# Optimization experiments

Hardware: AMD Instinct MI355X
Metric: run time of the kernel (lower is better)

The kernel has to match this reference:

```python
import jax, jax.numpy as jnp
import numpy as np

B, T, D = 16, 2048, 1024
TT = T - 2            # tokens after stripping BOS/EOS
WORD_EVERY = 3        # a word starts every 3 BPE tokens
MAX_WORDS = TT // WORD_EVERY  # 682
NUM_MUTEX, NUM_BIN = 64, 32


def setup_inputs() -> dict:
    key = jax.random.key(0)
    ks = jax.random.split(key, 7)
    features = jax.random.normal(ks[0], (B, T, D), dtype=jnp.float32)
    word_starts = jnp.zeros((B, TT), dtype=jnp.int32).at[:, ::WORD_EVERY].set(1)
    s = 1.0 / np.sqrt(D)
    dense_w = jax.random.normal(ks[1], (D, D), dtype=jnp.float32) * s
    dense_b = jax.random.normal(ks[2], (D,), dtype=jnp.float32) * 0.01
    out_w = jax.random.normal(ks[3], (NUM_MUTEX, D), dtype=jnp.float32) * s
    out_b = jax.random.normal(ks[4], (NUM_MUTEX,), dtype=jnp.float32) * 0.01
    bin_w = jax.random.normal(ks[5], (NUM_BIN, D + NUM_MUTEX), dtype=jnp.float32) * s
    bin_b = jax.random.normal(ks[6], (NUM_BIN,), dtype=jnp.float32) * 0.01
    return {"features": features, "word_starts": word_starts,
            "dense_w": dense_w, "dense_b": dense_b,
            "out_w": out_w, "out_b": out_b,
            "bin_w": bin_w, "bin_b": bin_b,
            "max_words": MAX_WORDS}


def _word_features(features, word_starts, max_words):
    # strip BOS/EOS
    x = features[:, 1:-1]                                  # [B, TT, D]
    b, tt, d = x.shape
    seg = jnp.cumsum(word_starts, axis=1) - 1              # word id per token; -1 before first start
    valid = seg >= 0
    flat_seg = seg + jnp.arange(b, dtype=seg.dtype)[:, None] * max_words
    overflow = b * max_words                               # dump invalid tokens into extra bucket
    flat_seg = jnp.where(valid, flat_seg, overflow).reshape(-1)
    sums = jax.ops.segment_sum(x.reshape(-1, d), flat_seg,
                               num_segments=b * max_words + 1)[:-1]
    counts = jax.ops.segment_sum(jnp.ones((b * tt,), dtype=x.dtype), flat_seg,
                                 num_segments=b * max_words + 1)[:-1]
    sums = sums.reshape(b, max_words, d)
    counts = counts.reshape(b, max_words, 1)
    # torch code initializes word_features to ONES; empty slots stay 1.0
    return jnp.where(counts > 0, sums, jnp.ones((), dtype=x.dtype))


def reference(features, word_starts, dense_w, dense_b, out_w, out_b, bin_w, bin_b, max_words):
    wf = _word_features(features, word_starts, max_words)   # [B, MW, D]
    # dropout p=0 (eval) -> identity
    h = jnp.tanh(jnp.einsum('bwd,ed->bwe', wf, dense_w) + dense_b)
    word_class_logits = jnp.einsum('bwd,cd->bwc', h, out_w) + out_b
    cat = jnp.concatenate((word_class_logits, h), axis=-1)  # [B, MW, Cm+D]
    binary_logits = jnp.einsum('bwd,cd->bwc', cat, bin_w) + bin_b
    return (word_class_logits, binary_logits)
```

## Files before the change

### kernel.cpp

```cpp
#include <hip/hip_runtime.h>
#include <stdint.h>

#define B_   16
#define T_   2048
#define D_   1024
#define TT_  2046
#define W_   682
#define BW_  (B_ * W_)
#define NMUT 64
#define NBIN 32

typedef __attribute__((ext_vector_type(8))) short s8b;
typedef __attribute__((ext_vector_type(4))) float f32x4;

__device__ inline short f2bf(float f) {
    uint32_t u = __builtin_bit_cast(uint32_t, f);
    u += 0x7FFFu + ((u >> 16) & 1u);
    return (short)(u >> 16);
}

__device__ inline void gload_lds16(const void* g, void* l) {
    __builtin_amdgcn_global_load_lds(
        (const __attribute__((address_space(1))) uint32_t*)g,
        (__attribute__((address_space(3))) uint32_t*)l, 16, 0, 0);
}

__global__ __launch_bounds__(256) void k_bounds(const int* __restrict__ ws,
                                                int* __restrict__ starts,
                                                int* __restrict__ nwords) {
    int b   = blockIdx.x;
    int tid = threadIdx.x;
    const int* row = ws + (size_t)b * TT_;

    int vals[8], incl[8];
    int p = 0;
    int t0 = tid * 8;
#pragma unroll
    for (int i = 0; i < 8; ++i) {
        int t = t0 + i;
        int v = (t < TT_) ? row[t] : 0;
        vals[i] = v;
        p += v;
        incl[i] = p;
    }
    int tot = p;

    int lane = tid & 63;
    int x = tot;
#pragma unroll
    for (int off = 1; off < 64; off <<= 1) {
        int v = __shfl_up(x, off);
        if (lane >= off) x += v;
    }

    __shared__ int wsum[4];
    int wid = tid >> 6;
    if (lane == 63) wsum[wid] = x;
    __syncthreads();

    int wbase = 0;
    for (int w = 0; w < wid; ++w) wbase += wsum[w];
    int excl = wbase + x - tot;

    int* st = starts + (size_t)b * (W_ + 1);
#pragma unroll
    for (int i = 0; i < 8; ++i) {
        if (vals[i]) {
            int w = excl + incl[i] - 1;
            if (w <= W_) st[w] = t0 + i;
        }
    }
    if (tid == 0) {
        int total = wsum[0] + wsum[1] + wsum[2] + wsum[3];
        int nw = total < W_ ? total : W_;
        nwords[b] = nw;
        if (total <= W_) st[total] = TT_;
    }
}

__global__ __launch_bounds__(256) void k_wf(const float* __restrict__ feat,
                                            const int* __restrict__ starts,
                                            const int* __restrict__ nwords,
                                            short* __restrict__ wf) {
    int blk = blockIdx.x;
    int b = blk / W_;
    int w = blk - b * W_;
    int tid = threadIdx.x;
    short* outp = wf + (size_t)blk * D_ + tid * 4;
    int nw = nwords[b];
    float4 acc = make_float4(0.f, 0.f, 0.f, 0.f);
    if (w >= nw) {
        acc = make_float4(1.f, 1.f, 1.f, 1.f);
    } else {
        const int* st = starts + (size_t)b * (W_ + 1);
        int s = st[w], e = st[w + 1];
        const float4* base = (const float4*)(feat + ((size_t)b * T_ + 1) * D_) + tid;
        for (int t = s; t < e; ++t) {
            float4 v = base[(size_t)t * (D_ / 4)];
            acc.x += v.x; acc.y += v.y; acc.z += v.z; acc.w += v.w;
        }
    }
    short4 o;
    o.x = f2bf(acc.x); o.y = f2bf(acc.y); o.z = f2bf(acc.z); o.w = f2bf(acc.w);
    *(short4*)outp = o;
}

__global__ __launch_bounds__(256) void k_cvt(const float* __restrict__ src,
                                             short* __restrict__ dst, int n4) {
    int i = blockIdx.x * 256 + threadIdx.x;
    if (i < n4) {
        float4 v = ((const float4*)src)[i];
        short4 o;
        o.x = f2bf(v.x); o.y = f2bf(v.y); o.z = f2bf(v.z); o.w = f2bf(v.w);
        *(short4*)(dst + (size_t)i * 4) = o;
    }
}

__global__ __launch_bounds__(256) void k_weff(const float* __restrict__ bin_w,
                                              const float* __restrict__ bin_b,
                                              const float* __restrict__ out_w,
                                              const float* __restrict__ out_b,
                                              short* __restrict__ Bcat,
                                              float* __restrict__ beff) {
    __shared__ float bc[NMUT];
    int j = blockIdx.x, tid = threadIdx.x;
    if (tid < NMUT) bc[tid] = bin_w[(size_t)j * (D_ + NMUT) + tid];
    __syncthreads();
    for (int k = tid; k < D_; k += 256) {
        float acc = bin_w[(size_t)j * (D_ + NMUT) + NMUT + k];
#pragma unroll 8
        for (int c = 0; c < NMUT; ++c)
            acc = fmaf(bc[c], out_w[(size_t)c * D_ + k], acc);
        Bcat[(size_t)(NMUT + j) * D_ + k] = f2bf(acc);
    }
    if (tid == 0) {
        float acc = bin_b[j];
        for (int c = 0; c < NMUT; ++c) acc = fmaf(bc[c], out_b[c], acc);
        beff[j] = acc;
    }
}

__global__ __launch_bounds__(256) void k_gemm1(const short* __restrict__ wf,
                                               const short* __restrict__ dwb,
                                               const float* __restrict__ db,
                                               short* __restrict__ h) {
    __shared__ short As[128 * 32];
    __shared__ short Bs[128 * 32];
    int tid  = threadIdx.x;
    int lane = tid & 63;
    int w    = tid >> 6;
    int wm = w >> 1, wn = w & 1;
    int bm = blockIdx.x * 128;
    int bn = blockIdx.y * 128;

    int ln = lane & 15;
    int qk = lane >> 4;

    int srow = lane >> 2;
    int scol = (lane & 3) * 8;

    f32x4 acc[4][4];
#pragma unroll
    for (int i = 0; i < 4; ++i)
#pragma unroll
        for (int j = 0; j < 4; ++j) acc[i][j] = (f32x4){0.f, 0.f, 0.f, 0.f};

    for (int kt = 0; kt < D_; kt += 32) {
#pragma unroll
        for (int p = 0; p < 2; ++p) {
            int chunk = w * 2 + p;
            int arow = bm + chunk * 16 + srow;
            arow = arow < BW_ ? arow : BW_ - 1;
            gload_lds16(wf + (size_t)arow * D_ + kt + scol, &As[chunk * 512]);
            int brow = bn + chunk * 16 + srow;
            gload_lds16(dwb + (size_t)brow * D_ + kt + scol, &Bs[chunk * 512]);
        }
        __syncthreads();
        s8b af[4], bf[4];
#pragma unroll
        for (int i = 0; i < 4; ++i)
            af[i] = *(const s8b*)&As[(wm * 64 + i * 16 + ln) * 32 + qk * 8];
#pragma unroll
        for (int j = 0; j < 4; ++j)
            bf[j] = *(const s8b*)&Bs[(wn * 64 + j * 16 + ln) * 32 + qk * 8];
#pragma unroll
        for (int i = 0; i < 4; ++i)
#pragma unroll
            for (int j = 0; j < 4; ++j)
                acc[i][j] = __builtin_amdgcn_mfma_f32_16x16x32_bf16(
                    af[i], bf[j], acc[i][j], 0, 0, 0);
        __syncthreads();
    }

    float bias[4];
#pragma unroll
    for (int j = 0; j < 4; ++j) bias[j] = db[bn + wn * 64 + j * 16 + ln];
#pragma unroll
    for (int i = 0; i < 4; ++i) {
        int row0 = bm + wm * 64 + i * 16 + qk * 4;
#pragma unroll
        for (int r = 0; r < 4; ++r) {
            int row = row0 + r;
            if (row < BW_) {
#pragma unroll
                for (int j = 0; j < 4; ++j) {
                    int cn = bn + wn * 64 + j * 16 + ln;
                    h[(size_t)row * D_ + cn] = f2bf(tanhf(acc[i][j][r] + bias[j]));
                }
            }
        }
    }
}

__global__ __launch_bounds__(256) void k_gemm2(const short* __restrict__ h,
                                               const short* __restrict__ Bcat,
                                               const float* __restrict__ ob,
                                               const float* __restrict__ beff,
                                               float* __restrict__ out) {
    __shared__ short As[64 * 32];
    int tid  = threadIdx.x;
    int lane = tid & 63;
    int w    = tid >> 6;
    int ln = lane & 15, qk = lane >> 4;
    int m0 = blockIdx.x * 64;
    int srow = lane >> 2, scol = (lane & 3) * 8;

    f32x4 acc[6];
#pragma unroll
    for (int j = 0; j < 6; ++j) acc[j] = (f32x4){0.f, 0.f, 0.f, 0.f};

    s8b bcur[6];
#pragma unroll
    for (int j = 0; j < 6; ++j)
        bcur[j] = *(const s8b*)(Bcat + (size_t)(j * 16 + ln) * D_ + qk * 8);

    for (int kt = 0; kt < D_; kt += 32) {
        int arow = m0 + w * 16 + srow;
        arow = arow < BW_ ? arow : BW_ - 1;
        gload_lds16(h + (size_t)arow * D_ + kt + scol, &As[w * 512]);
        __syncthreads();
        s8b af = *(const s8b*)&As[(w * 16 + ln) * 32 + qk * 8];
        int ktn = (kt + 32 < D_) ? kt + 32 : 0;
        s8b bnext[6];
#pragma unroll
        for (int j = 0; j < 6; ++j)
            bnext[j] = *(const s8b*)(Bcat + (size_t)(j * 16 + ln) * D_ + ktn + qk * 8);
#pragma unroll
        for (int j = 0; j < 6; ++j)
            acc[j] = __builtin_amdgcn_mfma_f32_16x16x32_bf16(af, bcur[j], acc[j], 0, 0, 0);
        __syncthreads();
#pragma unroll
        for (int j = 0; j < 6; ++j) bcur[j] = bnext[j];
    }

    float bj[6];
#pragma unroll
    for (int j = 0; j < 6; ++j) {
        int c = j * 16 + ln;
        bj[j] = (c < NMUT) ? ob[c] : beff[c - NMUT];
    }
#pragma unroll
    for (int r = 0; r < 4; ++r) {
        int row = m0 + w * 16 + qk * 4 + r;
        if (row < BW_) {
#pragma unroll
            for (int j = 0; j < 6; ++j) {
                int c = j * 16 + ln;
                float v = acc[j][r] + bj[j];
                if (c < NMUT) out[(size_t)row * NMUT + c] = v;
                else out[(size_t)BW_ * NMUT + (size_t)row * NBIN + (c - NMUT)] = v;
            }
        }
    }
}

extern "C" void kernel_launch(void* const* d_in, const int* in_sizes, int n_in,
                              void* d_out, int out_size, void* d_ws, size_t ws_size,
                              hipStream_t stream) {
    const float* feat    = (const float*)d_in[0];
    const int*   wstarts = (const int*)d_in[1];
    const float* dw      = (const float*)d_in[2];
    const float* db      = (const float*)d_in[3];
    const float* ow      = (const float*)d_in[4];
    const float* ob      = (const float*)d_in[5];
    const float* bw      = (const float*)d_in[6];
    const float* bb      = (const float*)d_in[7];
    float* out = (float*)d_out;

    char* ws = (char*)d_ws;
    size_t off = 0;
    auto alloc = [&](size_t bytes) {
        void* p = ws + off;
        off += (bytes + 255) & ~(size_t)255;
        return p;
    };
    short* wf     = (short*)alloc((size_t)BW_ * D_ * 2);
    short* h      = (short*)alloc((size_t)BW_ * D_ * 2);
    short* dwb    = (short*)alloc((size_t)D_ * D_ * 2);
    short* Bcat   = (short*)alloc((size_t)(NMUT + NBIN) * D_ * 2);
    float* beff   = (float*)alloc(NBIN * 4);
    int*   starts = (int*)alloc((size_t)B_ * (W_ + 1) * 4);
    int*   nwords = (int*)alloc(B_ * 4);

    k_bounds<<<B_, 256, 0, stream>>>(wstarts, starts, nwords);
    k_cvt<<<(D_ * D_ / 4 + 255) / 256, 256, 0, stream>>>(dw, dwb, D_ * D_ / 4);
    k_cvt<<<(NMUT * D_ / 4 + 255) / 256, 256, 0, stream>>>(ow, Bcat, NMUT * D_ / 4);
    k_weff<<<NBIN, 256, 0, stream>>>(bw, bb, ow, ob, Bcat, beff);
    k_wf<<<BW_, 256, 0, stream>>>(feat, starts, nwords, wf);
    k_gemm1<<<dim3((BW_ + 127) / 128, D_ / 128), 256, 0, stream>>>(wf, dwb, db, h);
    k_gemm2<<<(BW_ + 63) / 64, 256, 0, stream>>>(h, Bcat, ob, beff, out);
}
```

Before: 301.6 us.

## Merge prep kernels, double K-step in gemm1, fast tanh, direct-load gemm2

Folds the word-boundary scan, the two weight conversions and the effective binary-weight computation into one launch to cut launch overhead. gemm1 now loads 64-wide K slices per barrier pair, halving synchronisation, and uses an exp-based tanh in its epilogue. gemm2 drops LDS staging and barriers and loads A and B fragments straight from global memory. The fast tanh changes rounding slightly, and gemm2 leans on the cache for reuse.

```diff
diff --git a/kernel.cpp b/kernel.cpp
--- a/kernel.cpp
+++ b/kernel.cpp
@@ -19,62 +19,104 @@
     return (short)(u >> 16);
 }
 
+__device__ inline float fast_tanh(float x) {
+    float xc = fminf(fmaxf(x, -15.f), 15.f);
+    float e  = __expf(2.f * xc);
+    return 1.f - 2.f / (e + 1.f);
+}
+
 __device__ inline void gload_lds16(const void* g, void* l) {
     __builtin_amdgcn_global_load_lds(
         (const __attribute__((address_space(1))) uint32_t*)g,
         (__attribute__((address_space(3))) uint32_t*)l, 16, 0, 0);
 }
 
-__global__ __launch_bounds__(256) void k_bounds(const int* __restrict__ ws,
-                                                int* __restrict__ starts,
-                                                int* __restrict__ nwords) {
-    int b   = blockIdx.x;
+__global__ __launch_bounds__(256) void k_prep(const int* __restrict__ ws,
+                                              const float* __restrict__ dw,
+                                              const float* __restrict__ ow,
+                                              const float* __restrict__ ob,
+                                              const float* __restrict__ bw,
+                                              const float* __restrict__ bb,
+                                              int* __restrict__ starts,
+                                              int* __restrict__ nwords,
+                                              short* __restrict__ dwb,
+                                              short* __restrict__ Bcat,
+                                              float* __restrict__ beff) {
+    __shared__ float smem[NMUT];
+    int blk = blockIdx.x;
     int tid = threadIdx.x;
-    const int* row = ws + (size_t)b * TT_;
-
-    int vals[8], incl[8];
-    int p = 0;
-    int t0 = tid * 8;
-#pragma unroll
-    for (int i = 0; i < 8; ++i) {
-        int t = t0 + i;
-        int v = (t < TT_) ? row[t] : 0;
-        vals[i] = v;
-        p += v;
-        incl[i] = p;
-    }
-    int tot = p;
-
-    int lane = tid & 63;
-    int x = tot;
-#pragma unroll
-    for (int off = 1; off < 64; off <<= 1) {
-        int v = __shfl_up(x, off);
-        if (lane >= off) x += v;
-    }
-
-    __shared__ int wsum[4];
-    int wid = tid >> 6;
-    if (lane == 63) wsum[wid] = x;
-    __syncthreads();
-
-    int wbase = 0;
-    for (int w = 0; w < wid; ++w) wbase += wsum[w];
-    int excl = wbase + x - tot;
-
-    int* st = starts + (size_t)b * (W_ + 1);
-#pragma unroll
-    for (int i = 0; i < 8; ++i) {
-        if (vals[i]) {
-            int w = excl + incl[i] - 1;
-            if (w <= W_) st[w] = t0 + i;
-        }
-    }
-    if (tid == 0) {
-        int total = wsum[0] + wsum[1] + wsum[2] + wsum[3];
-        int nw = total < W_ ? total : W_;
-        nwords[b] = nw;
-        if (total <= W_) st[total] = TT_;
+
+    if (blk < 16) {
+        int b = blk;
+        const int* row = ws + (size_t)b * TT_;
+        int vals[8], incl[8];
+        int p = 0;
+        int t0 = tid * 8;
+#pragma unroll
+        for (int i = 0; i < 8; ++i) {
+            int t = t0 + i;
+            int v = (t < TT_) ? row[t] : 0;
+            vals[i] = v;
+            p += v;
+            incl[i] = p;
+        }
+        int tot = p;
+        int lane = tid & 63;
+        int x = tot;
+#pragma unroll
+        for (int off = 1; off < 64; off <<= 1) {
+            int v = __shfl_up(x, off);
+            if (lane >= off) x += v;
+        }
+        int* wsum = (int*)smem;
+        int wid = tid >> 6;
+        if (lane == 63) wsum[wid] = x;
+        __syncthreads();
+        int wbase = 0;
+        for (int q = 0; q < wid; ++q) wbase += wsum[q];
+        int excl = wbase + x - tot;
+        int* st = starts + (size_t)b * (W_ + 1);
+#pragma unroll
+        for (int i = 0; i < 8; ++i) {
+            if (vals[i]) {
+                int w = excl + incl[i] - 1;
+                if (w <= W_) st[w] = t0 + i;
+            }
+        }
+        if (tid == 0) {
+            int total = wsum[0] + wsum[1] + wsum[2] + wsum[3];
+            int nw = total < W_ ? total : W_;
+            nwords[b] = nw;
+            if (total <= W_) st[total] = TT_;
+        }
+    } else if (blk < 16 + 1024) {
+        int i = (blk - 16) * 256 + tid;
+        float4 v = ((const float4*)dw)[i];
+        short4 o;
+        o.x = f2bf(v.x); o.y = f2bf(v.y); o.z = f2bf(v.z); o.w = f2bf(v.w);
+        *(short4*)(dwb + (size_t)i * 4) = o;
+    } else if (blk < 16 + 1024 + 64) {
+        int i = (blk - 1040) * 256 + tid;
+        float4 v = ((const float4*)ow)[i];
+        short4 o;
+        o.x = f2bf(v.x); o.y = f2bf(v.y); o.z = f2bf(v.z); o.w = f2bf(v.w);
+        *(short4*)(Bcat + (size_t)i * 4) = o;
+    } else {
+        int j = blk - 1104;
+        if (tid < NMUT) smem[tid] = bw[(size_t)j * (D_ + NMUT) + tid];
+        __syncthreads();
+        for (int k = tid; k < D_; k += 256) {
+            float acc = bw[(size_t)j * (D_ + NMUT) + NMUT + k];
+#pragma unroll 8
+            for (int c = 0; c < NMUT; ++c)
+                acc = fmaf(smem[c], ow[(size_t)c * D_ + k], acc);
+            Bcat[(size_t)(NMUT + j) * D_ + k] = f2bf(acc);
+        }
+        if (tid == 0) {
+            float acc = bb[j];
+            for (int c = 0; c < NMUT; ++c) acc = fmaf(smem[c], ob[c], acc);
+            beff[j] = acc;
+        }
     }
 }
 
@@ -105,47 +147,12 @@
     *(short4*)outp = o;
 }
 
-__global__ __launch_bounds__(256) void k_cvt(const float* __restrict__ src,
-                                             short* __restrict__ dst, int n4) {
-    int i = blockIdx.x * 256 + threadIdx.x;
-    if (i < n4) {
-        float4 v = ((const float4*)src)[i];
-        short4 o;
-        o.x = f2bf(v.x); o.y = f2bf(v.y); o.z = f2bf(v.z); o.w = f2bf(v.w);
-        *(short4*)(dst + (size_t)i * 4) = o;
-    }
-}
-
-__global__ __launch_bounds__(256) void k_weff(const float* __restrict__ bin_w,
-                                              const float* __restrict__ bin_b,
-                                              const float* __restrict__ out_w,
-                                              const float* __restrict__ out_b,
-                                              short* __restrict__ Bcat,
-                                              float* __restrict__ beff) {
-    __shared__ float bc[NMUT];
-    int j = blockIdx.x, tid = threadIdx.x;
-    if (tid < NMUT) bc[tid] = bin_w[(size_t)j * (D_ + NMUT) + tid];
-    __syncthreads();
-    for (int k = tid; k < D_; k += 256) {
-        float acc = bin_w[(size_t)j * (D_ + NMUT) + NMUT + k];
-#pragma unroll 8
-        for (int c = 0; c < NMUT; ++c)
-            acc = fmaf(bc[c], out_w[(size_t)c * D_ + k], acc);
-        Bcat[(size_t)(NMUT + j) * D_ + k] = f2bf(acc);
-    }
-    if (tid == 0) {
-        float acc = bin_b[j];
-        for (int c = 0; c < NMUT; ++c) acc = fmaf(bc[c], out_b[c], acc);
-        beff[j] = acc;
-    }
-}
-
 __global__ __launch_bounds__(256) void k_gemm1(const short* __restrict__ wf,
                                                const short* __restrict__ dwb,
                                                const float* __restrict__ db,
                                                short* __restrict__ h) {
-    __shared__ short As[128 * 32];
-    __shared__ short Bs[128 * 32];
+    __shared__ short As[2][128 * 32];
+    __shared__ short Bs[2][128 * 32];
     int tid  = threadIdx.x;
     int lane = tid & 63;
     int w    = tid >> 6;
@@ -165,30 +172,38 @@
 #pragma unroll
         for (int j = 0; j < 4; ++j) acc[i][j] = (f32x4){0.f, 0.f, 0.f, 0.f};
 
-    for (int kt = 0; kt < D_; kt += 32) {
-#pragma unroll
-        for (int p = 0; p < 2; ++p) {
-            int chunk = w * 2 + p;
-            int arow = bm + chunk * 16 + srow;
-            arow = arow < BW_ ? arow : BW_ - 1;
-            gload_lds16(wf + (size_t)arow * D_ + kt + scol, &As[chunk * 512]);
-            int brow = bn + chunk * 16 + srow;
-            gload_lds16(dwb + (size_t)brow * D_ + kt + scol, &Bs[chunk * 512]);
+    for (int kt = 0; kt < D_; kt += 64) {
+#pragma unroll
+        for (int hh = 0; hh < 2; ++hh) {
+#pragma unroll
+            for (int p = 0; p < 2; ++p) {
+                int chunk = w * 2 + p;
+                int arow = bm + chunk * 16 + srow;
+                arow = arow < BW_ ? arow : BW_ - 1;
+                gload_lds16(wf + (size_t)arow * D_ + kt + hh * 32 + scol,
+                            &As[hh][chunk * 512]);
+                int brow = bn + chunk * 16 + srow;
+                gload_lds16(dwb + (size_t)brow * D_ + kt + hh * 32 + scol,
+                            &Bs[hh][chunk * 512]);
+            }
         }
         __syncthreads();
-        s8b af[4], bf[4];
-#pragma unroll
-        for (int i = 0; i < 4; ++i)
-            af[i] = *(const s8b*)&As[(wm * 64 + i * 16 + ln) * 32 + qk * 8];
-#pragma unroll
-        for (int j = 0; j < 4; ++j)
-            bf[j] = *(const s8b*)&Bs[(wn * 64 + j * 16 + ln) * 32 + qk * 8];
-#pragma unroll
-        for (int i = 0; i < 4; ++i)
+#pragma unroll
+        for (int hh = 0; hh < 2; ++hh) {
+            s8b af[4], bf[4];
+#pragma unroll
+            for (int i = 0; i < 4; ++i)
+                af[i] = *(const s8b*)&As[hh][(wm * 64 + i * 16 + ln) * 32 + qk * 8];
 #pragma unroll
             for (int j = 0; j < 4; ++j)
-                acc[i][j] = __builtin_amdgcn_mfma_f32_16x16x32_bf16(
-                    af[i], bf[j], acc[i][j], 0, 0, 0);
+                bf[j] = *(const s8b*)&Bs[hh][(wn * 64 + j * 16 + ln) * 32 + qk * 8];
+#pragma unroll
+            for (int i = 0; i < 4; ++i)
+#pragma unroll
+                for (int j = 0; j < 4; ++j)
+                    acc[i][j] = __builtin_amdgcn_mfma_f32_16x16x32_bf16(
+                        af[i], bf[j], acc[i][j], 0, 0, 0);
+        }
         __syncthreads();
     }
 
@@ -205,7 +220,8 @@
 #pragma unroll
                 for (int j = 0; j < 4; ++j) {
                     int cn = bn + wn * 64 + j * 16 + ln;
-                    h[(size_t)row * D_ + cn] = f2bf(tanhf(acc[i][j][r] + bias[j]));
+                    h[(size_t)row * D_ + cn] =
+                        f2bf(fast_tanh(acc[i][j][r] + bias[j]));
                 }
             }
         }
@@ -217,40 +233,31 @@
                                                const float* __restrict__ ob,
                                                const float* __restrict__ beff,
                                                float* __restrict__ out) {
-    __shared__ short As[64 * 32];
     int tid  = threadIdx.x;
     int lane = tid & 63;
     int w    = tid >> 6;
     int ln = lane & 15, qk = lane >> 4;
-    int m0 = blockIdx.x * 64;
-    int srow = lane >> 2, scol = (lane & 3) * 8;
+    int m0 = blockIdx.x * 64 + w * 16;
+
+    int arow = m0 + ln;
+    arow = arow < BW_ ? arow : BW_ - 1;
+    const short* ap = h + (size_t)arow * D_ + qk * 8;
+    const short* bp = Bcat + (size_t)ln * D_ + qk * 8;
 
     f32x4 acc[6];
 #pragma unroll
     for (int j = 0; j < 6; ++j) acc[j] = (f32x4){0.f, 0.f, 0.f, 0.f};
 
-    s8b bcur[6];
-#pragma unroll
-    for (int j = 0; j < 6; ++j)
-        bcur[j] = *(const s8b*)(Bcat + (size_t)(j * 16 + ln) * D_ + qk * 8);
-
+#pragma unroll 4
     for (int kt = 0; kt < D_; kt += 32) {
-        int arow = m0 + w * 16 + srow;
-        arow = arow < BW_ ? arow : BW_ - 1;
-        gload_lds16(h + (size_t)arow * D_ + kt + scol, &As[w * 512]);
-        __syncthreads();
-        s8b af = *(const s8b*)&As[(w * 16 + ln) * 32 + qk * 8];
-        int ktn = (kt + 32 < D_) ? kt + 32 : 0;
-        s8b bnext[6];
+        s8b af = *(const s8b*)(ap + kt);
+        s8b bf[6];
 #pragma unroll
         for (int j = 0; j < 6; ++j)
-            bnext[j] = *(const s8b*)(Bcat + (size_t)(j * 16 + ln) * D_ + ktn + qk * 8);
+            bf[j] = *(const s8b*)(bp + (size_t)j * 16 * D_ + kt);
 #pragma unroll
         for (int j = 0; j < 6; ++j)
-            acc[j] = __builtin_amdgcn_mfma_f32_16x16x32_bf16(af, bcur[j], acc[j], 0, 0, 0);
-        __syncthreads();
-#pragma unroll
-        for (int j = 0; j < 6; ++j) bcur[j] = bnext[j];
+            acc[j] = __builtin_amdgcn_mfma_f32_16x16x32_bf16(af, bf[j], acc[j], 0, 0, 0);
     }
 
     float bj[6];
@@ -261,7 +268,7 @@
     }
 #pragma unroll
     for (int r = 0; r < 4; ++r) {
-        int row = m0 + w * 16 + qk * 4 + r;
+        int row = m0 + qk * 4 + r;
         if (row < BW_) {
 #pragma unroll
             for (int j = 0; j < 6; ++j) {
@@ -302,10 +309,8 @@
     int*   starts = (int*)alloc((size_t)B_ * (W_ + 1) * 4);
     int*   nwords = (int*)alloc(B_ * 4);
 
-    k_bounds<<<B_, 256, 0, stream>>>(wstarts, starts, nwords);
-    k_cvt<<<(D_ * D_ / 4 + 255) / 256, 256, 0, stream>>>(dw, dwb, D_ * D_ / 4);
-    k_cvt<<<(NMUT * D_ / 4 + 255) / 256, 256, 0, stream>>>(ow, Bcat, NMUT * D_ / 4);
-    k_weff<<<NBIN, 256, 0, stream>>>(bw, bb, ow, ob, Bcat, beff);
+    k_prep<<<1136, 256, 0, stream>>>(wstarts, dw, ow, ob, bw, bb,
+                                     starts, nwords, dwb, Bcat, beff);
     k_wf<<<BW_, 256, 0, stream>>>(feat, starts, nwords, wf);
     k_gemm1<<<dim3((BW_ + 127) / 128, D_ / 128), 256, 0, stream>>>(wf, dwb, db, h);
     k_gemm2<<<(BW_ + 63) / 64, 256, 0, stream>>>(h, Bcat, ob, beff, out);
```

New measurement: 283.8 us. 5.9% less time.
